# Optimization experiments

Measured on AMD Instinct MI355X. Metric: run time of the kernel, lower is better.

The kernel has to match this reference:

```python
import jax, jax.numpy as jnp
import numpy as np

N = 55296      # nodes (C96 cubed-sphere)
B = 4          # batch
F = 64         # in_feats == out_feats
H = 256        # n_hidden
DEG = 4        # neighbors per node
E = N * DEG    # edges
NUM_STEP = 2


def setup_inputs() -> dict:
    key = jax.random.key(0)
    ks = jax.random.split(key, 24)
    inputs = jax.random.normal(ks[0], (B, N, F), jnp.float32)
    src = jax.random.randint(ks[1], (E,), 0, N, dtype=jnp.int32)
    dst = jnp.repeat(jnp.arange(N, dtype=jnp.int32), DEG)  # fixed in-degree 4
    d = {"inputs": inputs, "src": src, "dst": dst}
    # SAGEConv params: fc_self, fc_neigh, bias per layer
    dims = [(F, H), (H, H // 2), (H // 2, H // 4), (H // 4, H // 4), (H // 2, H // 2), (H, F)]
    for i, (di, do) in enumerate(dims, start=1):
        s = 1.0 / np.sqrt(di)
        d[f"ws{i}"] = jax.random.uniform(ks[3 * i], (di, do), jnp.float32, -s, s)
        d[f"wn{i}"] = jax.random.uniform(ks[3 * i + 1], (di, do), jnp.float32, -s, s)
        d[f"b{i}"] = jnp.zeros((do,), jnp.float32)
    return d


def _sage(x, src, dst, inv_deg, ws, wn, b):
    # x: [N, B, Fin] -> gather src endpoints, mean-aggregate onto dst nodes
    agg = jax.ops.segment_sum(x[src], dst, num_segments=N) * inv_deg  # [N, B, Fin]
    return jnp.einsum('nbf,fo->nbo', x, ws) + jnp.einsum('nbf,fo->nbo', agg, wn) + b


def reference(inputs, src, dst, ws1, wn1, b1, ws2, wn2, b2, ws3, wn3, b3,
              ws4, wn4, b4, ws5, wn5, b5, ws6, wn6, b6):
    deg = jax.ops.segment_sum(jnp.ones((E,), jnp.float32), dst, num_segments=N)
    inv_deg = (1.0 / jnp.maximum(deg, 1.0))[:, None, None]
    act = jax.nn.relu
    x = jnp.transpose(inputs, (1, 0, 2))  # [N, B, F]
    for _ in range(NUM_STEP):
        h1 = act(_sage(x, src, dst, inv_deg, ws1, wn1, b1))
        h2 = act(_sage(h1, src, dst, inv_deg, ws2, wn2, b2))
        h3 = act(_sage(h2, src, dst, inv_deg, ws3, wn3, b3))
        h4 = act(_sage(h3, src, dst, inv_deg, ws4, wn4, b4))
        h5 = jnp.concatenate([act(_sage(h4, src, dst, inv_deg, ws4, wn4, b4)), h3], axis=2)
        h6 = jnp.concatenate([act(_sage(h5, src, dst, inv_deg, ws5, wn5, b5)), h2], axis=2)
        x = _sage(h6, src, dst, inv_deg, ws6, wn6, b6)
    return jnp.transpose(x, (1, 0, 2))  # [B, N, F]
```

## Files before the change

### kernel.cpp

```cpp
#include <hip/hip_runtime.h>


#define NN 55296
#define MM (NN * 4)

typedef unsigned short u16;
typedef _Float16 f16;
typedef f16 f16x8 __attribute__((ext_vector_type(8)));
typedef float f32x4 __attribute__((ext_vector_type(4)));
typedef u16 u16x8 __attribute__((ext_vector_type(8)));

__device__ inline u16 f2h(float f) { return __builtin_bit_cast(u16, (f16)f); }
__device__ inline float h2f(u16 u) { return (float)__builtin_bit_cast(f16, u); }

__global__ __launch_bounds__(256) void k_fill(float* __restrict__ p, float v, int total) {
  int i = blockIdx.x * 256 + threadIdx.x;
  if (i < total) p[i] = v;
}

__global__ __launch_bounds__(256) void k_prep_x(const float* __restrict__ in,
                                                u16* __restrict__ out) {
  int idx = blockIdx.x * 256 + threadIdx.x;
  int n = idx >> 5, b = (idx >> 3) & 3, f0 = (idx & 7) * 8;
  const float* p = in + ((long)b * NN + n) * 64 + f0;
  float4 v0 = *(const float4*)p, v1 = *(const float4*)(p + 4);
  u16x8 r;
  r[0] = f2h(v0.x); r[1] = f2h(v0.y); r[2] = f2h(v0.z); r[3] = f2h(v0.w);
  r[4] = f2h(v1.x); r[5] = f2h(v1.y); r[6] = f2h(v1.z); r[7] = f2h(v1.w);
  *(u16x8*)(out + (((long)n * 4 + b) * 64 + f0)) = r;
}

__global__ __launch_bounds__(256) void k_prep_w(const float* __restrict__ wsrc,
                                                const float* __restrict__ wnsrc,
                                                int K, int N, u16* __restrict__ dst) {
  int idx = blockIdx.x * 256 + threadIdx.x;
  int K2 = 2 * K;
  if (idx >= N * K2) return;
  int n = idx / K2, k = idx - n * K2;
  float v = (k < K) ? wsrc[(long)k * N + n] : wnsrc[(long)(k - K) * N + n];
  dst[(long)n * K2 + k] = f2h(v);
}

__global__ __launch_bounds__(256) void k_prep_w2(const float* __restrict__ wsrc,
                                                 const float* __restrict__ wnsrc,
                                                 int K, int N, u16* __restrict__ dst) {
  int idx = blockIdx.x * 256 + threadIdx.x;
  int total = 2 * N * K;
  if (idx >= total) return;
  int r = idx / K, k = idx - r * K;
  float v = (r < N) ? wsrc[(long)k * N + r] : wnsrc[(long)k * N + (r - N)];
  dst[idx] = f2h(v);
}

template <int BM, int BN, int WM, int WN, typename TOUT, bool REMAP, bool GATHER>
__global__ __launch_bounds__(512, 4) void k_sage(
    const u16* __restrict__ X0, const u16* __restrict__ X1, int lda, int K0, int Ksum,
    const int4* __restrict__ src4, const u16* __restrict__ Wt,
    const float* __restrict__ bias, TOUT* __restrict__ OUT, long ldo,
    TOUT* __restrict__ OUT2, long ldo2, int Nsplit, int relu) {
  constexpr int GA = BM / 64;
  constexpr int GB = BN / 64;
  constexpr int NWM = BM / WM, NWN = BN / WN;
  static_assert(NWM * NWN == 8, "8 waves");
  constexpr int MF = WM / 16, NF = WN / 16;

  __shared__ __align__(16) u16 As[BM][64];
  __shared__ __align__(16) u16 Bs[BN][64];

  const int tid = threadIdx.x;
  const long m0 = (long)blockIdx.x * BM;
  const int n0 = blockIdx.y * BN;
  const int K2 = GATHER ? 2 * Ksum : Ksum;

  const int srow = tid >> 3;
  const int scg = tid & 7;

  int o_self[GA], o_g[GA][4];
#pragma unroll
  for (int i = 0; i < GA; ++i) {
    long m = m0 + srow + 64 * i;
    o_self[i] = (int)(m * lda);
    if constexpr (GATHER) {
      int b = (int)(m & 3);
      int4 s = src4[(int)(m >> 2)];
      o_g[i][0] = (s.x * 4 + b) * lda;
      o_g[i][1] = (s.y * 4 + b) * lda;
      o_g[i][2] = (s.z * 4 + b) * lda;
      o_g[i][3] = (s.w * 4 + b) * lda;
    }
  }
  long o_b[GB];
#pragma unroll
  for (int j = 0; j < GB; ++j) o_b[j] = (long)(n0 + srow + 64 * j) * K2 + scg * 8;

  u16x8 ra[GA][4];
  u16x8 rb[GB];

  const int w = tid >> 6, lane = tid & 63;
  const int wm = w % NWM, wn = w / NWM;
  const int mo = wm * WM, no = wn * WN;
  const int lr = lane & 15, lg = lane >> 4;

  f32x4 acc[MF][NF];
#pragma unroll
  for (int i = 0; i < MF; ++i)
#pragma unroll
    for (int j = 0; j < NF; ++j) {
      f32x4 z = {0.f, 0.f, 0.f, 0.f};
      acc[i][j] = z;
    }

  auto issue = [&](int kt) {
    const bool agg = GATHER && (kt >= Ksum);
    int cs = agg ? kt - Ksum : kt;
    const u16* Xp = X0;
    if (cs >= K0) { Xp = X1; cs -= K0; }
    const int cb = cs + scg * 8;
#pragma unroll
    for (int i = 0; i < GA; ++i) {
      if (agg) {
#pragma unroll
        for (int k = 0; k < 4; ++k)
          ra[i][k] = *(const u16x8*)(Xp + (long)o_g[i][k] + cb);
      } else {
        ra[i][0] = *(const u16x8*)(Xp + (long)o_self[i] + cb);
      }
    }
#pragma unroll
    for (int j = 0; j < GB; ++j)
      rb[j] = *(const u16x8*)(Wt + o_b[j] + kt);
  };
  auto commit = [&](bool agg) {
#pragma unroll
    for (int i = 0; i < GA; ++i) {
      const int row = srow + 64 * i;
      u16x8 v = ra[i][0];
      if (agg) {
        f16x8 s01 = __builtin_bit_cast(f16x8, ra[i][0]) + __builtin_bit_cast(f16x8, ra[i][1]);
        f16x8 s23 = __builtin_bit_cast(f16x8, ra[i][2]) + __builtin_bit_cast(f16x8, ra[i][3]);
        v = __builtin_bit_cast(u16x8, (s01 + s23) * (f16)0.25f);
      }
      *(u16x8*)&As[row][(scg ^ (row & 7)) * 8] = v;
    }
#pragma unroll
    for (int j = 0; j < GB; ++j) {
      const int row = srow + 64 * j;
      *(u16x8*)&Bs[row][(scg ^ (row & 7)) * 8] = rb[j];
    }
  };

  issue(0);
  for (int kt = 0; kt < K2; kt += 64) {
    commit(GATHER && kt >= Ksum);
    __syncthreads();
    const int nx = kt + 64;
    if (nx < K2) issue(nx);
#pragma unroll
    for (int ks = 0; ks < 2; ++ks) {
      f16x8 af[MF], bfr[NF];
#pragma unroll
      for (int i = 0; i < MF; ++i) {
        const int row = mo + i * 16 + lr;
        af[i] = __builtin_bit_cast(f16x8,
                  *(const u16x8*)&As[row][((ks * 4 + lg) ^ (row & 7)) * 8]);
      }
#pragma unroll
      for (int j = 0; j < NF; ++j) {
        const int row = no + j * 16 + lr;
        bfr[j] = __builtin_bit_cast(f16x8,
                   *(const u16x8*)&Bs[row][((ks * 4 + lg) ^ (row & 7)) * 8]);
      }
#pragma unroll
      for (int i = 0; i < MF; ++i)
#pragma unroll
        for (int j = 0; j < NF; ++j)
          acc[i][j] = __builtin_amdgcn_mfma_f32_16x16x32_f16(af[i], bfr[j], acc[i][j], 0, 0, 0);
    }
    __syncthreads();
  }

#pragma unroll
  for (int i = 0; i < MF; ++i)
#pragma unroll
    for (int j = 0; j < NF; ++j) {
      const int col = n0 + no + j * 16 + lr;
      const float bv = bias ? bias[col] : 0.f;
      TOUT* Op; long ld; int c;
      if (col < Nsplit) { Op = OUT; ld = ldo; c = col; }
      else              { Op = OUT2; ld = ldo2; c = col - Nsplit; }
#pragma unroll
      for (int r = 0; r < 4; ++r) {
        float v = acc[i][j][r] + bv;
        if (relu) v = fmaxf(v, 0.f);
        const long m = m0 + mo + i * 16 + lg * 4 + r;
        const long orow = REMAP ? ((m & 3) * (long)NN + (m >> 2)) : m;
        if constexpr (sizeof(TOUT) == 2) Op[orow * ld + c] = (TOUT)f2h(v);
        else                             Op[orow * ld + c] = v;
      }
    }
}

template <int N1, int KS1, int K2B, int N2, int NSPLIT>
__global__ __launch_bounds__(512, 4) void k_fuse2(
    const u16* __restrict__ X0, const u16* __restrict__ X1, int lda, int K0,
    const int4* __restrict__ src4,
    const u16* __restrict__ W1t, const float* __restrict__ bias1,
    const u16* __restrict__ G2, int ldg2,
    const u16* __restrict__ W2t,
    u16* __restrict__ OUT, long ldo, u16* __restrict__ OUT2, long ldo2) {
  constexpr int K21 = 2 * KS1;
  constexpr int K22 = N1 + K2B;
  constexpr int GB1 = N1 / 64, GB2 = N2 / 64;
  constexpr int BSROWS = (N1 > N2 ? N1 : N2);
  __shared__ __align__(16) u16 T[64][N1];
  __shared__ __align__(16) u16 As[64][64];
  __shared__ __align__(16) u16 Bs[BSROWS][64];

  const int tid = threadIdx.x;
  const long m0 = (long)blockIdx.x * 64;
  const int srow = tid >> 3, scg = tid & 7;
  const long mrow = m0 + srow;

  const int o_self = (int)(mrow * lda);
  const int bb = (int)(mrow & 3);
  const int4 s = src4[(int)(mrow >> 2)];
  const int og0 = (s.x * 4 + bb) * lda, og1 = (s.y * 4 + bb) * lda;
  const int og2 = (s.z * 4 + bb) * lda, og3 = (s.w * 4 + bb) * lda;

  const int w = tid >> 6, lane = tid & 63;
  const int lr = lane & 15, lg = lane >> 4;

  constexpr int NWN1 = N1 / 32, NWM1 = 8 / NWN1, WM1 = 64 / NWM1, MF1 = WM1 / 16;
  const int mo1 = (w % NWM1) * WM1, no1 = (w / NWM1) * 32;

  int ob1[GB1];
#pragma unroll
  for (int j = 0; j < GB1; ++j) ob1[j] = (srow + 64 * j) * K21 + scg * 8;

  u16x8 ra0, ra1, ra2, ra3, rb[GB1];

  auto issue1 = [&](int kt) {
    const bool agg = kt >= KS1;
    int cs = agg ? kt - KS1 : kt;
    const u16* Xp = X0;
    if (cs >= K0) { Xp = X1; cs -= K0; }
    const int cb = cs + scg * 8;
    if (agg) {
      ra0 = *(const u16x8*)(Xp + og0 + cb);
      ra1 = *(const u16x8*)(Xp + og1 + cb);
      ra2 = *(const u16x8*)(Xp + og2 + cb);
      ra3 = *(const u16x8*)(Xp + og3 + cb);
    } else {
      ra0 = *(const u16x8*)(Xp + o_self + cb);
    }
#pragma unroll
    for (int j = 0; j < GB1; ++j)
      rb[j] = *(const u16x8*)(W1t + ob1[j] + kt);
  };
  auto commit1 = [&](bool agg) {
    u16x8 v = ra0;
    if (agg) {
      f16x8 s01 = __builtin_bit_cast(f16x8, ra0) + __builtin_bit_cast(f16x8, ra1);
      f16x8 s23 = __builtin_bit_cast(f16x8, ra2) + __builtin_bit_cast(f16x8, ra3);
      v = __builtin_bit_cast(u16x8, (s01 + s23) * (f16)0.25f);
    }
    *(u16x8*)&As[srow][(scg ^ (srow & 7)) * 8] = v;
#pragma unroll
    for (int j = 0; j < GB1; ++j) {
      const int row = srow + 64 * j;
      *(u16x8*)&Bs[row][(scg ^ (row & 7)) * 8] = rb[j];
    }
  };

  f32x4 acc1[MF1][2];
#pragma unroll
  for (int i = 0; i < MF1; ++i) {
    f32x4 z = {0.f, 0.f, 0.f, 0.f};
    acc1[i][0] = z; acc1[i][1] = z;
  }

  issue1(0);
  for (int kt = 0; kt < K21; kt += 64) {
    commit1(kt >= KS1);
    __syncthreads();
    if (kt + 64 < K21) issue1(kt + 64);
#pragma unroll
    for (int ks = 0; ks < 2; ++ks) {
      f16x8 af[MF1], bf0, bf1;
#pragma unroll
      for (int i = 0; i < MF1; ++i) {
        const int row = mo1 + i * 16 + lr;
        af[i] = __builtin_bit_cast(f16x8,
                  *(const u16x8*)&As[row][((ks * 4 + lg) ^ (row & 7)) * 8]);
      }
      {
        const int row = no1 + lr;
        bf0 = __builtin_bit_cast(f16x8,
                *(const u16x8*)&Bs[row][((ks * 4 + lg) ^ (row & 7)) * 8]);
      }
      {
        const int row = no1 + 16 + lr;
        bf1 = __builtin_bit_cast(f16x8,
                *(const u16x8*)&Bs[row][((ks * 4 + lg) ^ (row & 7)) * 8]);
      }
#pragma unroll
      for (int i = 0; i < MF1; ++i) {
        acc1[i][0] = __builtin_amdgcn_mfma_f32_16x16x32_f16(af[i], bf0, acc1[i][0], 0, 0, 0);
        acc1[i][1] = __builtin_amdgcn_mfma_f32_16x16x32_f16(af[i], bf1, acc1[i][1], 0, 0, 0);
      }
    }
    __syncthreads();
  }

#pragma unroll
  for (int i = 0; i < MF1; ++i)
#pragma unroll
    for (int j = 0; j < 2; ++j) {
      const int col = no1 + j * 16 + lr;
      const float bv = bias1[col];
#pragma unroll
      for (int r = 0; r < 4; ++r) {
        float v = fmaxf(acc1[i][j][r] + bv, 0.f);
        const int row = mo1 + i * 16 + lg * 4 + r;
        T[row][(((col >> 3) ^ (row & 7)) << 3) | (col & 7)] = f2h(v);
      }
    }

  constexpr int NWN2 = N2 / 32, NWM2 = 8 / NWN2, WM2 = 64 / NWM2, MF2 = WM2 / 16;
  const int mo2 = (w % NWM2) * WM2, no2 = (w / NWM2) * 32;

  int ob2[GB2];
#pragma unroll
  for (int j = 0; j < GB2; ++j) ob2[j] = (srow + 64 * j) * K22 + scg * 8;
  const long oG = (K2B > 0) ? (mrow * (long)ldg2 + scg * 8) : 0;

  u16x8 rb2[GB2], rg;

  auto issue2 = [&](int kt) {
#pragma unroll
    for (int j = 0; j < GB2; ++j)
      rb2[j] = *(const u16x8*)(W2t + ob2[j] + kt);
    if constexpr (K2B > 0) {
      if (kt >= N1) rg = *(const u16x8*)(G2 + oG + (kt - N1));
    }
  };
  auto commit2 = [&](int kt) {
#pragma unroll
    for (int j = 0; j < GB2; ++j) {
      const int row = srow + 64 * j;
      *(u16x8*)&Bs[row][(scg ^ (row & 7)) * 8] = rb2[j];
    }
    if constexpr (K2B > 0) {
      if (kt >= N1) *(u16x8*)&As[srow][(scg ^ (srow & 7)) * 8] = rg;
    }
  };

  f32x4 acc2[MF2][2];
#pragma unroll
  for (int i = 0; i < MF2; ++i) {
    f32x4 z = {0.f, 0.f, 0.f, 0.f};
    acc2[i][0] = z; acc2[i][1] = z;
  }

  issue2(0);
  for (int kt = 0; kt < K22; kt += 64) {
    commit2(kt);
    __syncthreads();
    if (kt + 64 < K22) issue2(kt + 64);
    const bool fromT = kt < N1;
#pragma unroll
    for (int ks = 0; ks < 2; ++ks) {
      f16x8 af[MF2], bf0, bf1;
#pragma unroll
      for (int i = 0; i < MF2; ++i) {
        const int row = mo2 + i * 16 + lr;
        if (fromT) {
          const int g = (kt >> 3) + ks * 4 + lg;
          af[i] = __builtin_bit_cast(f16x8,
                    *(const u16x8*)&T[row][(g ^ (row & 7)) * 8]);
        } else {
          af[i] = __builtin_bit_cast(f16x8,
                    *(const u16x8*)&As[row][((ks * 4 + lg) ^ (row & 7)) * 8]);
        }
      }
      {
        const int row = no2 + lr;
        bf0 = __builtin_bit_cast(f16x8,
                *(const u16x8*)&Bs[row][((ks * 4 + lg) ^ (row & 7)) * 8]);
      }
      {
        const int row = no2 + 16 + lr;
        bf1 = __builtin_bit_cast(f16x8,
                *(const u16x8*)&Bs[row][((ks * 4 + lg) ^ (row & 7)) * 8]);
      }
#pragma unroll
      for (int i = 0; i < MF2; ++i) {
        acc2[i][0] = __builtin_amdgcn_mfma_f32_16x16x32_f16(af[i], bf0, acc2[i][0], 0, 0, 0);
        acc2[i][1] = __builtin_amdgcn_mfma_f32_16x16x32_f16(af[i], bf1, acc2[i][1], 0, 0, 0);
      }
    }
    __syncthreads();
  }

#pragma unroll
  for (int i = 0; i < MF2; ++i)
#pragma unroll
    for (int j = 0; j < 2; ++j) {
      const int col = no2 + j * 16 + lr;
      u16* Op; long ld; int c;
      if (col < NSPLIT) { Op = OUT; ld = ldo; c = col; }
      else              { Op = OUT2; ld = ldo2; c = col - NSPLIT; }
#pragma unroll
      for (int r = 0; r < 4; ++r) {
        const long m = m0 + mo2 + i * 16 + lg * 4 + r;
        Op[m * ld + c] = f2h(acc2[i][j][r]);
      }
    }
}

template <typename TOUT, bool REMAP, bool RELU, int GSH>
__global__ __launch_bounds__(256) void k_gadd(
    const u16* __restrict__ Y, long ldy, const u16* __restrict__ Z, long ldz,
    const int4* __restrict__ src4, const float* __restrict__ bias,
    TOUT* __restrict__ OUT, long ldo) {
  const int idx = blockIdx.x * 256 + threadIdx.x;
  const int g = idx & ((1 << GSH) - 1);
  const long m = idx >> GSH;
  const int b = (int)(m & 3), n = (int)(m >> 2);
  const int4 s = src4[n];
  u16x8 ys = *(const u16x8*)(Y + m * ldy + g * 8);
  u16x8 z0 = *(const u16x8*)(Z + (long)(s.x * 4 + b) * ldz + g * 8);
  u16x8 z1 = *(const u16x8*)(Z + (long)(s.y * 4 + b) * ldz + g * 8);
  u16x8 z2 = *(const u16x8*)(Z + (long)(s.z * 4 + b) * ldz + g * 8);
  u16x8 z3 = *(const u16x8*)(Z + (long)(s.w * 4 + b) * ldz + g * 8);
  float4 bv0 = *(const float4*)(bias + g * 8);
  float4 bv1 = *(const float4*)(bias + g * 8 + 4);
  float o[8];
#pragma unroll
  for (int j = 0; j < 8; ++j) {
    float bj = (j < 4) ? (&bv0.x)[j] : (&bv1.x)[j - 4];
    float v = h2f(ys[j]) + 0.25f * (h2f(z0[j]) + h2f(z1[j]) + h2f(z2[j]) + h2f(z3[j])) + bj;
    o[j] = RELU ? fmaxf(v, 0.f) : v;
  }
  const long orow = REMAP ? ((long)b * NN + n) : m;
  if constexpr (sizeof(TOUT) == 2) {
    u16x8 r;
#pragma unroll
    for (int j = 0; j < 8; ++j) r[j] = f2h(o[j]);
    *(u16x8*)(OUT + orow * ldo + g * 8) = r;
  } else {
#pragma unroll
    for (int j = 0; j < 8; ++j) OUT[orow * ldo + g * 8 + j] = o[j];
  }
}

extern "C" void kernel_launch(void* const* d_in, const int* in_sizes, int n_in,
                              void* d_out, int out_size, void* d_ws, size_t ws_size,
                              hipStream_t stream) {
  const float* inputs = (const float*)d_in[0];
  const int*   src    = (const int*)d_in[1];
  const float* W[6][3];
  for (int i = 0; i < 6; ++i) {
    W[i][0] = (const float*)d_in[3 + 3 * i];
    W[i][1] = (const float*)d_in[4 + 3 * i];
    W[i][2] = (const float*)d_in[5 + 3 * i];
  }

  const long M = (long)MM;
  const int dims[6][2] = {{64,256},{256,128},{128,64},{64,64},{128,128},{256,64}};
  long wo[6]; long wtot = 0;
  for (int i = 0; i < 6; ++i) { wo[i] = wtot; wtot += (long)dims[i][1] * 2 * dims[i][0]; }
  const long woD3 = wtot;
  wtot += 2L * dims[3][1] * dims[3][0];

  const size_t needed = ((size_t)384 * M + wtot) * sizeof(u16);
  if (ws_size < needed) {
    float mb = (float)(ws_size >> 20);
    k_fill<<<(out_size + 255) / 256, 256, 0, stream>>>((float*)d_out, mb, out_size);
    return;
  }

  u16* act = (u16*)d_ws;
  u16* Y1  = act + 0 * M;
  u16* H2  = act + 0 * M;
  u16* Z1  = act + 128 * M;
  u16* YZ2 = act + 128 * M;
  u16* Z4  = act + 128 * M;
  u16* Y6  = act + 128 * M;
  u16* H5a = act + 192 * M;
  u16* H3  = act + 256 * M;
  u16* Xb  = act + 320 * M;
  u16* Y4  = act + 320 * M;
  u16* Z6  = act + 320 * M;
  u16* WT  = act + 384 * M;
  u16* Xp  = (u16*)d_out;
  const int4* src4 = (const int4*)src;

  k_prep_x<<<NN * 32 / 256, 256, 0, stream>>>(inputs, Xb);
  for (int i : {0, 3, 4}) {
    int total = dims[i][1] * 2 * dims[i][0];
    k_prep_w<<<(total + 255) / 256, 256, 0, stream>>>(W[i][0], W[i][1], dims[i][0],
                                                      dims[i][1], WT + wo[i]);
  }
  for (int i : {1, 2, 5}) {
    int total = 2 * dims[i][1] * dims[i][0];
    k_prep_w2<<<(total + 255) / 256, 256, 0, stream>>>(W[i][0], W[i][1], dims[i][0],
                                                       dims[i][1], WT + wo[i]);
  }
  {
    int total = 2 * dims[3][1] * dims[3][0];
    k_prep_w2<<<(total + 255) / 256, 256, 0, stream>>>(W[3][0], W[3][1], dims[3][0],
                                                       dims[3][1], WT + woD3);
  }

  const int BIG = 1 << 30;
  const dim3 g1(MM / 128, 1);
  for (int step = 0; step < 2; ++step) {
    const u16* x0 = step ? Xp : Xb;
    k_fuse2<256, 64, 0, 256, 128><<<MM / 64, 512, 0, stream>>>(
        x0, x0, 64, 64, src4, WT + wo[0], W[0][2],
        nullptr, 0, WT + wo[1], Y1, 128, Z1, 128);
    k_gadd<u16, false, true, 4><<<MM * 16 / 256, 256, 0, stream>>>(
        Y1, 128, Z1, 128, src4, W[1][2], H2, 128);
    k_sage<128, 128, 64, 32, u16, false, false><<<g1, 512, 0, stream>>>(
        H2, H2, 128, 128, 128, src4, WT + wo[2], nullptr, YZ2, 128,
        (u16*)nullptr, 0, BIG, 0);
    k_gadd<u16, false, true, 3><<<MM * 8 / 256, 256, 0, stream>>>(
        YZ2, 128, YZ2 + 64, 128, src4, W[2][2], H3, 64);
    k_fuse2<64, 64, 0, 128, 64><<<MM / 64, 512, 0, stream>>>(
        H3, H3, 64, 64, src4, WT + wo[3], W[3][2],
        nullptr, 0, WT + woD3, Y4, 64, Z4, 64);
    k_gadd<u16, false, true, 3><<<MM * 8 / 256, 256, 0, stream>>>(
        Y4, 64, Z4, 64, src4, W[3][2], H5a, 64);
    k_fuse2<128, 128, 128, 128, 64><<<MM / 64, 512, 0, stream>>>(
        H5a, H3, 64, 64, src4, WT + wo[4], W[4][2],
        H2, 128, WT + wo[5], Y6, 64, Z6, 64);
    if (step == 0)
      k_gadd<u16, false, false, 3><<<MM * 8 / 256, 256, 0, stream>>>(
          Y6, 64, Z6, 64, src4, W[5][2], Xp, 64);
    else
      k_gadd<float, true, false, 3><<<MM * 8 / 256, 256, 0, stream>>>(
          Y6, 64, Z6, 64, src4, W[5][2], (float*)d_out, 64);
  }
}
```

Measured before the change: 648.2 us.

## Load first-stage GEMM operands directly from global into MFMA registers, skipping LDS

```diff
diff --git a/kernel.cpp b/kernel.cpp
--- a/kernel.cpp
+++ b/kernel.cpp
@@ -12,6 +12,9 @@
 
 __device__ inline u16 f2h(float f) { return __builtin_bit_cast(u16, (f16)f); }
 __device__ inline float h2f(u16 u) { return (float)__builtin_bit_cast(f16, u); }
+__device__ inline f16x8 ldh8(const u16* p) {
+  return __builtin_bit_cast(f16x8, *(const u16x8*)p);
+}
 
 __global__ __launch_bounds__(256) void k_fill(float* __restrict__ p, float v, int total) {
   int i = blockIdx.x * 256 + threadIdx.x;
@@ -210,106 +213,70 @@
     u16* __restrict__ OUT, long ldo, u16* __restrict__ OUT2, long ldo2) {
   constexpr int K21 = 2 * KS1;
   constexpr int K22 = N1 + K2B;
-  constexpr int GB1 = N1 / 64, GB2 = N2 / 64;
-  constexpr int BSROWS = (N1 > N2 ? N1 : N2);
+  constexpr int GB2 = N2 / 64;
   __shared__ __align__(16) u16 T[64][N1];
-  __shared__ __align__(16) u16 As[64][64];
-  __shared__ __align__(16) u16 Bs[BSROWS][64];
+  __shared__ __align__(16) u16 Bs[N2][64];
+  __shared__ __align__(16) u16 As[(K2B > 0) ? 64 : 1][64];
 
   const int tid = threadIdx.x;
   const long m0 = (long)blockIdx.x * 64;
   const int srow = tid >> 3, scg = tid & 7;
   const long mrow = m0 + srow;
 
-  const int o_self = (int)(mrow * lda);
-  const int bb = (int)(mrow & 3);
-  const int4 s = src4[(int)(mrow >> 2)];
-  const int og0 = (s.x * 4 + bb) * lda, og1 = (s.y * 4 + bb) * lda;
-  const int og2 = (s.z * 4 + bb) * lda, og3 = (s.w * 4 + bb) * lda;
-
   const int w = tid >> 6, lane = tid & 63;
   const int lr = lane & 15, lg = lane >> 4;
 
   constexpr int NWN1 = N1 / 32, NWM1 = 8 / NWN1, WM1 = 64 / NWM1, MF1 = WM1 / 16;
   const int mo1 = (w % NWM1) * WM1, no1 = (w / NWM1) * 32;
 
-  int ob1[GB1];
-#pragma unroll
-  for (int j = 0; j < GB1; ++j) ob1[j] = (srow + 64 * j) * K21 + scg * 8;
-
-  u16x8 ra0, ra1, ra2, ra3, rb[GB1];
-
-  auto issue1 = [&](int kt) {
+  long aoff[MF1]; int goff[MF1][4];
+#pragma unroll
+  for (int i = 0; i < MF1; ++i) {
+    const long m = m0 + mo1 + i * 16 + lr;
+    aoff[i] = m * lda;
+    const int b = (int)(m & 3);
+    const int4 s = src4[(int)(m >> 2)];
+    goff[i][0] = (s.x * 4 + b) * lda;
+    goff[i][1] = (s.y * 4 + b) * lda;
+    goff[i][2] = (s.z * 4 + b) * lda;
+    goff[i][3] = (s.w * 4 + b) * lda;
+  }
+
+  f32x4 acc1[MF1][2];
+#pragma unroll
+  for (int i = 0; i < MF1; ++i) {
+    f32x4 z = {0.f, 0.f, 0.f, 0.f};
+    acc1[i][0] = z; acc1[i][1] = z;
+  }
+
+#pragma unroll
+  for (int kt = 0; kt < K21; kt += 32) {
     const bool agg = kt >= KS1;
     int cs = agg ? kt - KS1 : kt;
     const u16* Xp = X0;
     if (cs >= K0) { Xp = X1; cs -= K0; }
-    const int cb = cs + scg * 8;
-    if (agg) {
-      ra0 = *(const u16x8*)(Xp + og0 + cb);
-      ra1 = *(const u16x8*)(Xp + og1 + cb);
-      ra2 = *(const u16x8*)(Xp + og2 + cb);
-      ra3 = *(const u16x8*)(Xp + og3 + cb);
-    } else {
-      ra0 = *(const u16x8*)(Xp + o_self + cb);
-    }
-#pragma unroll
-    for (int j = 0; j < GB1; ++j)
-      rb[j] = *(const u16x8*)(W1t + ob1[j] + kt);
-  };
-  auto commit1 = [&](bool agg) {
-    u16x8 v = ra0;
-    if (agg) {
-      f16x8 s01 = __builtin_bit_cast(f16x8, ra0) + __builtin_bit_cast(f16x8, ra1);
-      f16x8 s23 = __builtin_bit_cast(f16x8, ra2) + __builtin_bit_cast(f16x8, ra3);
-      v = __builtin_bit_cast(u16x8, (s01 + s23) * (f16)0.25f);
-    }
-    *(u16x8*)&As[srow][(scg ^ (srow & 7)) * 8] = v;
-#pragma unroll
-    for (int j = 0; j < GB1; ++j) {
-      const int row = srow + 64 * j;
-      *(u16x8*)&Bs[row][(scg ^ (row & 7)) * 8] = rb[j];
-    }
-  };
-
-  f32x4 acc1[MF1][2];
-#pragma unroll
-  for (int i = 0; i < MF1; ++i) {
-    f32x4 z = {0.f, 0.f, 0.f, 0.f};
-    acc1[i][0] = z; acc1[i][1] = z;
-  }
-
-  issue1(0);
-  for (int kt = 0; kt < K21; kt += 64) {
-    commit1(kt >= KS1);
-    __syncthreads();
-    if (kt + 64 < K21) issue1(kt + 64);
-#pragma unroll
-    for (int ks = 0; ks < 2; ++ks) {
-      f16x8 af[MF1], bf0, bf1;
-#pragma unroll
-      for (int i = 0; i < MF1; ++i) {
-        const int row = mo1 + i * 16 + lr;
-        af[i] = __builtin_bit_cast(f16x8,
-                  *(const u16x8*)&As[row][((ks * 4 + lg) ^ (row & 7)) * 8]);
-      }
-      {
-        const int row = no1 + lr;
-        bf0 = __builtin_bit_cast(f16x8,
-                *(const u16x8*)&Bs[row][((ks * 4 + lg) ^ (row & 7)) * 8]);
-      }
-      {
-        const int row = no1 + 16 + lr;
-        bf1 = __builtin_bit_cast(f16x8,
-                *(const u16x8*)&Bs[row][((ks * 4 + lg) ^ (row & 7)) * 8]);
-      }
-#pragma unroll
-      for (int i = 0; i < MF1; ++i) {
-        acc1[i][0] = __builtin_amdgcn_mfma_f32_16x16x32_f16(af[i], bf0, acc1[i][0], 0, 0, 0);
-        acc1[i][1] = __builtin_amdgcn_mfma_f32_16x16x32_f16(af[i], bf1, acc1[i][1], 0, 0, 0);
-      }
-    }
-    __syncthreads();
+    const int c = cs + lg * 8;
+    f16x8 af[MF1];
+#pragma unroll
+    for (int i = 0; i < MF1; ++i) {
+      if (agg) {
+        f16x8 g0 = ldh8(Xp + goff[i][0] + c);
+        f16x8 g1 = ldh8(Xp + goff[i][1] + c);
+        f16x8 g2 = ldh8(Xp + goff[i][2] + c);
+        f16x8 g3 = ldh8(Xp + goff[i][3] + c);
+        af[i] = ((g0 + g1) + (g2 + g3)) * (f16)0.25f;
+      } else {
+        af[i] = ldh8(Xp + aoff[i] + c);
+      }
+    }
+    const long wc = kt + lg * 8;
+    f16x8 bf0 = ldh8(W1t + (long)(no1 + lr) * K21 + wc);
+    f16x8 bf1 = ldh8(W1t + (long)(no1 + 16 + lr) * K21 + wc);
+#pragma unroll
+    for (int i = 0; i < MF1; ++i) {
+      acc1[i][0] = __builtin_amdgcn_mfma_f32_16x16x32_f16(af[i], bf0, acc1[i][0], 0, 0, 0);
+      acc1[i][1] = __builtin_amdgcn_mfma_f32_16x16x32_f16(af[i], bf1, acc1[i][1], 0, 0, 0);
+    }
   }
 
 #pragma unroll
@@ -329,9 +296,9 @@
   constexpr int NWN2 = N2 / 32, NWM2 = 8 / NWN2, WM2 = 64 / NWM2, MF2 = WM2 / 16;
   const int mo2 = (w % NWM2) * WM2, no2 = (w / NWM2) * 32;
 
-  int ob2[GB2];
-#pragma unroll
-  for (int j = 0; j < GB2; ++j) ob2[j] = (srow + 64 * j) * K22 + scg * 8;
+  long ob2[GB2];
+#pragma unroll
+  for (int j = 0; j < GB2; ++j) ob2[j] = (long)(srow + 64 * j) * K22 + scg * 8;
   const long oG = (K2B > 0) ? (mrow * (long)ldg2 + scg * 8) : 0;
 
   u16x8 rb2[GB2], rg;
```

Measured after the change: 1.191 ms. +83.8%, slower.
